# Kernel optimization log

Hardware: AMD Instinct MI355X
Metric: run time of the kernel (lower is better)

## Reference

```python
import jax, jax.numpy as jnp
import numpy as np

N, E, IN_DIM, HID, OUT = 50000, 800000, 256, 128, 128
EPS_BN = 1e-5
EPS_NORM = 1e-12


def leaky(x):
    return jnp.where(x >= 0, x, 0.2 * x)


def batchnorm(x, gamma, beta):
    # training-mode BatchNorm1d over node dimension
    mean = jnp.mean(x, axis=0)
    var = jnp.var(x, axis=0)
    return gamma * (x - mean) * jax.lax.rsqrt(var + EPS_BN) + beta


def sage_conv(x, src, dst, W_l, b_l, W_r):
    # PyG SAGEConv (mean aggr): lin_l(mean_{j->i} x_j) + lin_r(x_i)
    msg = x[src]  # [E, D] gather
    agg = jax.ops.segment_sum(msg, dst, num_segments=N)
    cnt = jax.ops.segment_sum(jnp.ones((E,), x.dtype), dst, num_segments=N)
    agg = agg / jnp.maximum(cnt, 1.0)[:, None]
    return agg @ W_l + b_l + x @ W_r


def setup_inputs() -> dict:
    key = jax.random.key(0)
    ks = jax.random.split(key, 16)
    s = lambda fan_in: (2.0 / fan_in) ** 0.5
    return {
        "x": jax.random.normal(ks[0], (N, IN_DIM), jnp.float32),
        "edge_index": jax.random.randint(ks[1], (2, E), 0, N),
        "W_in": jax.random.normal(ks[2], (IN_DIM, HID), jnp.float32) * s(IN_DIM),
        "b_in": jnp.zeros((HID,), jnp.float32),
        "g1": jnp.ones((HID,), jnp.float32),
        "be1": jnp.zeros((HID,), jnp.float32),
        "Wl1": jax.random.normal(ks[3], (HID, HID), jnp.float32) * s(HID),
        "bl1": jnp.zeros((HID,), jnp.float32),
        "Wr1": jax.random.normal(ks[4], (HID, HID), jnp.float32) * s(HID),
        "Wl2": jax.random.normal(ks[5], (HID, OUT), jnp.float32) * s(HID),
        "bl2": jnp.zeros((OUT,), jnp.float32),
        "Wr2": jax.random.normal(ks[6], (HID, OUT), jnp.float32) * s(HID),
        "Wskip": jax.random.normal(ks[7], (HID, OUT), jnp.float32) * s(HID),
        "bskip": jnp.zeros((OUT,), jnp.float32),
        "g2": jnp.ones((OUT,), jnp.float32),
        "be2": jnp.zeros((OUT,), jnp.float32),
    }


def reference(x, edge_index, W_in, b_in, g1, be1, Wl1, bl1, Wr1, Wl2, bl2, Wr2, Wskip, bskip, g2, be2):
    src, dst = edge_index[0], edge_index[1]
    h = batchnorm(leaky(x @ W_in + b_in), g1, be1)
    skip = h
    h1 = leaky(sage_conv(h, src, dst, Wl1, bl1, Wr1))  # dropout = identity (eval)
    h2 = sage_conv(h1, src, dst, Wl2, bl2, Wr2)
    out = h2 + (skip @ Wskip + bskip)
    out = batchnorm(out, g2, be2)
    norm = jnp.sqrt(jnp.sum(out * out, axis=1, keepdims=True))
    return out / jnp.maximum(norm, EPS_NORM)
```

## Files before the change

### kernel.cpp

```cpp
#include <hip/hip_runtime.h>
#include <math.h>

#define N_NODES 50000
#define N_EDGES 800000
#define IN_DIM 256
#define HID 128
#define ZPITCH 384

typedef unsigned short u16;
typedef u16 u16x8 __attribute__((ext_vector_type(8)));
typedef u16 u16x2 __attribute__((ext_vector_type(2)));
typedef __bf16 bf16x8 __attribute__((ext_vector_type(8)));
typedef float f32x4 __attribute__((ext_vector_type(4)));

union F8 { u16x8 u; bf16x8 h; };

__device__ __forceinline__ u16 f2b(float f) {
    unsigned u = __builtin_bit_cast(unsigned, f);
    u = (u + 0x7FFFu + ((u >> 16) & 1u)) >> 16;
    return (u16)u;
}
__device__ __forceinline__ float b2f(u16 h) {
    unsigned u = ((unsigned)h) << 16;
    return __builtin_bit_cast(float, u);
}

template<int A_F32>
__device__ __forceinline__ F8 load_a(const void* base, size_t row, int P, int koff)
{
    F8 r;
    if (A_F32) {
        const float* p = (const float*)base + row * P + koff;
        float4 f0 = *reinterpret_cast<const float4*>(p);
        float4 f1 = *reinterpret_cast<const float4*>(p + 4);
        r.h[0] = (__bf16)f0.x; r.h[1] = (__bf16)f0.y;
        r.h[2] = (__bf16)f0.z; r.h[3] = (__bf16)f0.w;
        r.h[4] = (__bf16)f1.x; r.h[5] = (__bf16)f1.y;
        r.h[6] = (__bf16)f1.z; r.h[7] = (__bf16)f1.w;
    } else {
        r.u = *reinterpret_cast<const u16x8*>((const u16*)base + row * P + koff);
    }
    return r;
}

template<int LEAKY, int STATS, int OUT_BF16, int A_F32>
__global__ __launch_bounds__(256) void gemm_mfma(
    int M, const void* __restrict__ A, int P, int K,
    const u16* __restrict__ Wf,
    const float* __restrict__ bias0, const float* __restrict__ bias1,
    void* __restrict__ Cout, int CP,
    float* __restrict__ stats)
{
    const int t   = threadIdx.x;
    const int w   = t >> 6;
    const int l   = t & 63;
    const int l15 = l & 15;
    const int lg  = l >> 4;
    const int rb  = blockIdx.x * 64 + w * 16;

    int r0 = rb + l15;
    size_t r0c = (size_t)(r0 < M ? r0 : M - 1);
    const int ko = lg * 8;
    const u16* pb = Wf + l * 8;

    f32x4 acc[8];
#pragma unroll
    for (int j = 0; j < 8; ++j) acc[j] = 0.0f;

    F8 a0, b[8];
    a0 = load_a<A_F32>(A, r0c, P, ko);
#pragma unroll
    for (int j = 0; j < 8; ++j) b[j].u = *(const u16x8*)(pb + j * 512);

    const int NC = K >> 5;
    for (int c = 1; c < NC; ++c) {
        F8 na0, nb[8];
        na0 = load_a<A_F32>(A, r0c, P, c * 32 + ko);
#pragma unroll
        for (int j = 0; j < 8; ++j) nb[j].u = *(const u16x8*)(pb + c * 4096 + j * 512);
#pragma unroll
        for (int j = 0; j < 8; ++j)
            acc[j] = __builtin_amdgcn_mfma_f32_16x16x32_bf16(a0.h, b[j].h, acc[j], 0, 0, 0);
        a0 = na0;
#pragma unroll
        for (int j = 0; j < 8; ++j) b[j] = nb[j];
    }
#pragma unroll
    for (int j = 0; j < 8; ++j)
        acc[j] = __builtin_amdgcn_mfma_f32_16x16x32_bf16(a0.h, b[j].h, acc[j], 0, 0, 0);

    float bias_j[8];
#pragma unroll
    for (int j = 0; j < 8; ++j) {
        float bb = bias0[16 * j + l15];
        if (bias1) bb += bias1[16 * j + l15];
        bias_j[j] = bb;
    }

    float csum[8], csq[8];
#pragma unroll
    for (int j = 0; j < 8; ++j) { csum[j] = 0.f; csq[j] = 0.f; }

    {
        int rbase = rb + lg * 4;
#pragma unroll
        for (int r = 0; r < 4; ++r) {
            int row = rbase + r;
            bool ok = row < M;
#pragma unroll
            for (int j = 0; j < 8; ++j) {
                float y = acc[j][r] + bias_j[j];
                if (LEAKY) y = (y >= 0.f) ? y : 0.2f * y;
                if (ok) {
                    if (OUT_BF16)
                        ((u16*)Cout)[(size_t)row * CP + 16 * j + l15] = f2b(y);
                    else
                        ((float*)Cout)[(size_t)row * CP + 16 * j + l15] = y;
                    if (STATS) { csum[j] += y; csq[j] += y * y; }
                }
            }
        }
    }

    if (STATS) {
        __shared__ float sred[256];
        sred[t] = 0.f;
        __syncthreads();
#pragma unroll
        for (int j = 0; j < 8; ++j) {
            float s = csum[j];
            float q = csq[j];
            s += __shfl_xor(s, 16); s += __shfl_xor(s, 32);
            q += __shfl_xor(q, 16); q += __shfl_xor(q, 32);
            if (lg == 0) {
                atomicAdd(&sred[16 * j + l15], s);
                atomicAdd(&sred[128 + 16 * j + l15], q);
            }
        }
        __syncthreads();
        atomicAdd(&stats[t], sred[t]);
    }
}

__global__ __launch_bounds__(256) void conv_w(const float* s0, const float* s1, const float* s2,
                                              const float* sc0, const float* sc1, const float* sc2,
                                              int rows_each, u16* __restrict__ dst, int nchunks)
{
    int tid = blockIdx.x * 256 + threadIdx.x;
    if (tid >= nchunks * 512) return;
    int c   = tid >> 9;
    int j   = (tid >> 6) & 7;
    int l   = tid & 63;
    int l15 = l & 15, lg = l >> 4;

    int srow0 = c * 32;
    int si    = srow0 / rows_each;
    const float* S  = (si == 0) ? s0 : (si == 1) ? s1 : s2;
    const float* SC = (si == 0) ? sc0 : (si == 1) ? sc1 : sc2;
    int rbase = srow0 - si * rows_each + lg * 8;
    int col   = 16 * j + l15;

    u16x8 o;
#pragma unroll
    for (int i = 0; i < 8; ++i) {
        float v = S[(size_t)(rbase + i) * HID + col];
        if (SC) v *= SC[rbase + i];
        o[i] = f2b(v);
    }
    reinterpret_cast<u16x8*>(dst)[tid] = o;
}

__global__ void bias_fold(const float* __restrict__ b0, const float* __restrict__ b1,
                          const float* __restrict__ W0, const float* __restrict__ W1,
                          const float* __restrict__ sh, float* __restrict__ outb)
{
    int j = threadIdx.x;
    float acc = b0[j] + (b1 ? b1[j] : 0.f);
    for (int i = 0; i < HID; ++i) {
        float w = W0[(size_t)i * HID + j] + (W1 ? W1[(size_t)i * HID + j] : 0.f);
        acc = fmaf(sh[i], w, acc);
    }
    outb[j] = acc;
}

__global__ void bn_params(const float* __restrict__ stats,
                          const float* __restrict__ gamma,
                          const float* __restrict__ beta,
                          float* __restrict__ scale,
                          float* __restrict__ shift, float invn)
{
    int j = threadIdx.x;
    float mean = stats[j] * invn;
    float var  = stats[128 + j] * invn - mean * mean;
    var = fmaxf(var, 0.f);
    float sc = gamma[j] / sqrtf(var + 1e-5f);
    scale[j] = sc;
    shift[j] = beta[j] - mean * sc;
}

__global__ __launch_bounds__(256) void edge_count(const int* __restrict__ dst, int* __restrict__ cnt)
{
    int e = blockIdx.x * 256 + threadIdx.x;
    if (e < N_EDGES) atomicAdd(&cnt[dst[e]], 1);
}

__global__ __launch_bounds__(256) void scan_block(const int* __restrict__ cnt,
                                                  int* __restrict__ excl,
                                                  int* __restrict__ bsum, int n)
{
    __shared__ int sh[256];
    int t = threadIdx.x;
    int i = blockIdx.x * 256 + t;
    int v = (i < n) ? cnt[i] : 0;
    sh[t] = v;
    __syncthreads();
#pragma unroll
    for (int off = 1; off < 256; off <<= 1) {
        int x = (t >= off) ? sh[t - off] : 0;
        __syncthreads();
        sh[t] += x;
        __syncthreads();
    }
    if (i < n) excl[i] = sh[t] - v;
    if (t == 255) bsum[blockIdx.x] = sh[255];
}

__global__ __launch_bounds__(256) void scan_bsum(int* __restrict__ bsum, int nb)
{
    __shared__ int sh[256];
    int t = threadIdx.x;
    int v = (t < nb) ? bsum[t] : 0;
    sh[t] = v;
    __syncthreads();
#pragma unroll
    for (int off = 1; off < 256; off <<= 1) {
        int x = (t >= off) ? sh[t - off] : 0;
        __syncthreads();
        sh[t] += x;
        __syncthreads();
    }
    if (t < nb) bsum[t] = sh[t] - v;
}

__global__ __launch_bounds__(256) void scan_add(int* __restrict__ row_ptr,
                                                int* __restrict__ fillrp,
                                                const int* __restrict__ bsum, int n)
{
    int i = blockIdx.x * 256 + threadIdx.x;
    if (i < n) {
        int v = row_ptr[i] + bsum[i >> 8];
        row_ptr[i] = v;
        fillrp[i]  = v;
    }
    if (i == 0) row_ptr[n] = N_EDGES;
}

#define FILL_EPB 4096
__global__ __launch_bounds__(256) void edge_fill_part(const int* __restrict__ src,
                                                      const int* __restrict__ dst,
                                                      int* __restrict__ fillrp,
                                                      int* __restrict__ col_idx)
{
    const int range = blockIdx.x & 7;
    const int base  = (blockIdx.x >> 3) * FILL_EPB;
    const int lo = range * 6250, hi = lo + 6250;
#pragma unroll
    for (int k = 0; k < FILL_EPB / 256; ++k) {
        int e = base + k * 256 + threadIdx.x;
        if (e < N_EDGES) {
            int d = dst[e];
            if (d >= lo && d < hi) {
                int pos = atomicAdd(&fillrp[d], 1);
                col_idx[pos] = src[e];
            }
        }
    }
}

__global__ __launch_bounds__(256) void spmm_mean(const int* __restrict__ row_ptr,
                                                 const int* __restrict__ col_idx,
                                                 const u16* __restrict__ Z_in,
                                                 u16* __restrict__ Z_out)
{
    int node = blockIdx.x * 4 + (threadIdx.x >> 6);
    if (node >= N_NODES) return;
    int lane = threadIdx.x & 63;
    int beg = row_ptr[node];
    int end = row_ptr[node + 1];

    float sx = 0.f, sy = 0.f;
    int e = beg;
    for (; e + 4 <= end; e += 4) {
        int c0 = col_idx[e], c1 = col_idx[e + 1], c2 = col_idx[e + 2], c3 = col_idx[e + 3];
        u16x2 v0 = *reinterpret_cast<const u16x2*>(Z_in + (size_t)c0 * ZPITCH + lane * 2);
        u16x2 v1 = *reinterpret_cast<const u16x2*>(Z_in + (size_t)c1 * ZPITCH + lane * 2);
        u16x2 v2 = *reinterpret_cast<const u16x2*>(Z_in + (size_t)c2 * ZPITCH + lane * 2);
        u16x2 v3 = *reinterpret_cast<const u16x2*>(Z_in + (size_t)c3 * ZPITCH + lane * 2);
        sx += (b2f(v0[0]) + b2f(v1[0])) + (b2f(v2[0]) + b2f(v3[0]));
        sy += (b2f(v0[1]) + b2f(v1[1])) + (b2f(v2[1]) + b2f(v3[1]));
    }
    for (; e < end; ++e) {
        int c = col_idx[e];
        u16x2 v = *reinterpret_cast<const u16x2*>(Z_in + (size_t)c * ZPITCH + lane * 2);
        sx += b2f(v[0]); sy += b2f(v[1]);
    }
    float inv = 1.f / fmaxf((float)(end - beg), 1.f);
    u16x2 r; r[0] = f2b(sx * inv); r[1] = f2b(sy * inv);
    *reinterpret_cast<u16x2*>(Z_out + (size_t)node * ZPITCH + lane * 2) = r;
}

__global__ __launch_bounds__(256) void bn_rownorm(float* __restrict__ out,
                                                  const float* __restrict__ scale,
                                                  const float* __restrict__ shift)
{
    int row = blockIdx.x * 4 + (threadIdx.x >> 6);
    if (row >= N_NODES) return;
    int lane = threadIdx.x & 63;
    float2 v  = *reinterpret_cast<const float2*>(&out[(size_t)row * HID + lane * 2]);
    float2 sc = *reinterpret_cast<const float2*>(&scale[lane * 2]);
    float2 sh = *reinterpret_cast<const float2*>(&shift[lane * 2]);
    float y0 = v.x * sc.x + sh.x;
    float y1 = v.y * sc.y + sh.y;
    float ss = y0 * y0 + y1 * y1;
#pragma unroll
    for (int m = 1; m < 64; m <<= 1) ss += __shfl_xor(ss, m);
    float inv = 1.f / fmaxf(sqrtf(ss), 1e-12f);
    float2 r = {y0 * inv, y1 * inv};
    *reinterpret_cast<float2*>(&out[(size_t)row * HID + lane * 2]) = r;
}

extern "C" void kernel_launch(void* const* d_in, const int* in_sizes, int n_in,
                              void* d_out, int out_size, void* d_ws, size_t ws_size,
                              hipStream_t stream)
{
    const float* x     = (const float*)d_in[0];
    const int*   ei    = (const int*)d_in[1];
    const float* W_in  = (const float*)d_in[2];
    const float* b_in  = (const float*)d_in[3];
    const float* g1    = (const float*)d_in[4];
    const float* be1   = (const float*)d_in[5];
    const float* Wl1   = (const float*)d_in[6];
    const float* bl1   = (const float*)d_in[7];
    const float* Wr1   = (const float*)d_in[8];
    const float* Wl2   = (const float*)d_in[9];
    const float* bl2   = (const float*)d_in[10];
    const float* Wr2   = (const float*)d_in[11];
    const float* Wskip = (const float*)d_in[12];
    const float* bskip = (const float*)d_in[13];
    const float* g2    = (const float*)d_in[14];
    const float* be2   = (const float*)d_in[15];
    float* out = (float*)d_out;

    char* ws = (char*)d_ws;
    u16*  Z  = (u16*)ws;
    char* zzone = ws + 38400000;
    float* stats = (float*)zzone;
    int*   icnt  = (int*)(zzone + 2048);
    size_t zsz   = 2048 + (size_t)N_NODES * 4;
    int*   row_ptr = (int*)(zzone + zsz);
    int*   fillrp  = (int*)(zzone + zsz + 200064);
    int*   bsum    = (int*)(zzone + zsz + 400128);
    int*   col_idx = (int*)(zzone + zsz + 400128 + 1024);
    float* bnc     = (float*)(zzone + zsz + 400128 + 1024 + (size_t)N_EDGES * 4);
    u16* WfA = (u16*)((char*)bnc + 4096);
    u16* WfB = WfA + 8 * 4096;
    u16* WfC = WfB + 8 * 4096;

    hipMemsetAsync(zzone, 0, zsz, stream);

    const int* srcp = ei;
    const int* dstp = ei + N_EDGES;

    float* scale1 = bnc;
    float* shift1 = bnc + 128;
    float* scale2 = bnc + 256;
    float* shift2 = bnc + 384;
    float* b1eff  = bnc + 512;
    float* b2eff  = bnc + 640;

    conv_w<<<16, 256, 0, stream>>>(W_in, nullptr, nullptr, nullptr, nullptr, nullptr,
                                   256, WfA, 8);

    const int NB = (N_NODES + 255) / 256;
    edge_count<<<(N_EDGES + 255) / 256, 256, 0, stream>>>(dstp, icnt);
    scan_block<<<NB, 256, 0, stream>>>(icnt, row_ptr, bsum, N_NODES);
    scan_bsum<<<1, 256, 0, stream>>>(bsum, NB);
    scan_add<<<NB, 256, 0, stream>>>(row_ptr, fillrp, bsum, N_NODES);
    edge_fill_part<<<((N_EDGES + FILL_EPB - 1) / FILL_EPB) * 8, 256, 0, stream>>>(
        srcp, dstp, fillrp, col_idx);

    const int GB = (N_NODES + 63) / 64;

    gemm_mfma<1, 1, 1, 1><<<GB, 256, 0, stream>>>(
        N_NODES, x, IN_DIM, 256, WfA, b_in, nullptr, Z + 128, ZPITCH, stats);
    bn_params<<<1, 128, 0, stream>>>(stats, g1, be1, scale1, shift1, 1.f / N_NODES);

    conv_w<<<16, 256, 0, stream>>>(Wl1, Wr1, nullptr, scale1, scale1, nullptr,
                                   128, WfB, 8);
    conv_w<<<24, 256, 0, stream>>>(Wl2, Wskip, Wr2, nullptr, scale1, nullptr,
                                   128, WfC, 12);
    bias_fold<<<1, 128, 0, stream>>>(bl1, nullptr, Wl1, Wr1, shift1, b1eff);
    bias_fold<<<1, 128, 0, stream>>>(bl2, bskip, Wskip, nullptr, shift1, b2eff);

    spmm_mean<<<(N_NODES + 3) / 4, 256, 0, stream>>>(row_ptr, col_idx, Z + 128, Z);
    gemm_mfma<1, 0, 1, 0><<<GB, 256, 0, stream>>>(
        N_NODES, Z, ZPITCH, 256, WfB, b1eff, nullptr, Z + 256, ZPITCH, nullptr);

    spmm_mean<<<(N_NODES + 3) / 4, 256, 0, stream>>>(row_ptr, col_idx, Z + 256, Z);
    gemm_mfma<0, 1, 0, 0><<<GB, 256, 0, stream>>>(
        N_NODES, Z, ZPITCH, 384, WfC, b2eff, nullptr, out, HID, stats + 256);

    bn_params<<<1, 128, 0, stream>>>(stats + 256, g2, be2, scale2, shift2, 1.f / N_NODES);
    bn_rownorm<<<(N_NODES + 3) / 4, 256, 0, stream>>>(out, scale2, shift2);
}
```

Baseline: 314.9 us.

## Stage packed weights in LDS and preload all A fragments in MFMA GEMM

The GEMM kernel now copies the whole packed weight matrix into shared memory once per block, and each wave reads its B fragments from LDS instead of global memory. Blocks grow to 512 threads covering 128 rows, and the K-loop is unrolled at compile time with all A fragments loaded up front. This cuts redundant global and L2 reads of the weights and exposes more memory-level parallelism. The cost is up to 96KB of LDS and more registers, which may limit occupancy, plus a block-wide sync before compute.

```diff
diff --git a/kernel.cpp b/kernel.cpp
--- a/kernel.cpp
+++ b/kernel.cpp
@@ -43,51 +43,51 @@
     return r;
 }
 
-template<int LEAKY, int STATS, int OUT_BF16, int A_F32>
-__global__ __launch_bounds__(256) void gemm_mfma(
-    int M, const void* __restrict__ A, int P, int K,
+template<int LEAKY, int STATS, int OUT_BF16, int A_F32, int NC>
+__global__ __launch_bounds__(512, 3) void gemm_mfma(
+    int M, const void* __restrict__ A, int P,
     const u16* __restrict__ Wf,
     const float* __restrict__ bias0, const float* __restrict__ bias1,
     void* __restrict__ Cout, int CP,
     float* __restrict__ stats)
 {
+    __shared__ u16 Bs[NC * 4096];
+
     const int t   = threadIdx.x;
     const int w   = t >> 6;
     const int l   = t & 63;
     const int l15 = l & 15;
     const int lg  = l >> 4;
-    const int rb  = blockIdx.x * 64 + w * 16;
+    const int rb  = blockIdx.x * 128 + w * 16;
 
     int r0 = rb + l15;
     size_t r0c = (size_t)(r0 < M ? r0 : M - 1);
     const int ko = lg * 8;
-    const u16* pb = Wf + l * 8;
+
+    F8 a[NC];
+#pragma unroll
+    for (int c = 0; c < NC; ++c) a[c] = load_a<A_F32>(A, r0c, P, c * 32 + ko);
+
+#pragma unroll
+    for (int i = 0; i < NC; ++i) {
+        int idx = i * 512 + t;
+        reinterpret_cast<u16x8*>(Bs)[idx] = reinterpret_cast<const u16x8*>(Wf)[idx];
+    }
+    __syncthreads();
 
     f32x4 acc[8];
 #pragma unroll
     for (int j = 0; j < 8; ++j) acc[j] = 0.0f;
 
-    F8 a0, b[8];
-    a0 = load_a<A_F32>(A, r0c, P, ko);
-#pragma unroll
-    for (int j = 0; j < 8; ++j) b[j].u = *(const u16x8*)(pb + j * 512);
-
-    const int NC = K >> 5;
-    for (int c = 1; c < NC; ++c) {
-        F8 na0, nb[8];
-        na0 = load_a<A_F32>(A, r0c, P, c * 32 + ko);
-#pragma unroll
-        for (int j = 0; j < 8; ++j) nb[j].u = *(const u16x8*)(pb + c * 4096 + j * 512);
-#pragma unroll
-        for (int j = 0; j < 8; ++j)
-            acc[j] = __builtin_amdgcn_mfma_f32_16x16x32_bf16(a0.h, b[j].h, acc[j], 0, 0, 0);
-        a0 = na0;
-#pragma unroll
-        for (int j = 0; j < 8; ++j) b[j] = nb[j];
-    }
-#pragma unroll
-    for (int j = 0; j < 8; ++j)
-        acc[j] = __builtin_amdgcn_mfma_f32_16x16x32_bf16(a0.h, b[j].h, acc[j], 0, 0, 0);
+#pragma unroll
+    for (int c = 0; c < NC; ++c) {
+#pragma unroll
+        for (int j = 0; j < 8; ++j) {
+            F8 b;
+            b.u = reinterpret_cast<const u16x8*>(Bs)[(c * 8 + j) * 64 + l];
+            acc[j] = __builtin_amdgcn_mfma_f32_16x16x32_bf16(a[c].h, b.h, acc[j], 0, 0, 0);
+        }
+    }
 
     float bias_j[8];
 #pragma unroll
@@ -124,7 +124,7 @@
 
     if (STATS) {
         __shared__ float sred[256];
-        sred[t] = 0.f;
+        if (t < 256) sred[t] = 0.f;
         __syncthreads();
 #pragma unroll
         for (int j = 0; j < 8; ++j) {
@@ -138,7 +138,7 @@
             }
         }
         __syncthreads();
-        atomicAdd(&stats[t], sred[t]);
+        if (t < 256) atomicAdd(&stats[t], sred[t]);
     }
 }
 
@@ -389,10 +389,10 @@
     edge_fill_part<<<((N_EDGES + FILL_EPB - 1) / FILL_EPB) * 8, 256, 0, stream>>>(
         srcp, dstp, fillrp, col_idx);
 
-    const int GB = (N_NODES + 63) / 64;
-
-    gemm_mfma<1, 1, 1, 1><<<GB, 256, 0, stream>>>(
-        N_NODES, x, IN_DIM, 256, WfA, b_in, nullptr, Z + 128, ZPITCH, stats);
+    const int GB = (N_NODES + 127) / 128;
+
+    gemm_mfma<1, 1, 1, 1, 8><<<GB, 512, 0, stream>>>(
+        N_NODES, x, IN_DIM, WfA, b_in, nullptr, Z + 128, ZPITCH, stats);
     bn_params<<<1, 128, 0, stream>>>(stats, g1, be1, scale1, shift1, 1.f / N_NODES);
 
     conv_w<<<16, 256, 0, stream>>>(Wl1, Wr1, nullptr, scale1, scale1, nullptr,
@@ -403,12 +403,12 @@
     bias_fold<<<1, 128, 0, stream>>>(bl2, bskip, Wskip, nullptr, shift1, b2eff);
 
     spmm_mean<<<(N_NODES + 3) / 4, 256, 0, stream>>>(row_ptr, col_idx, Z + 128, Z);
-    gemm_mfma<1, 0, 1, 0><<<GB, 256, 0, stream>>>(
-        N_NODES, Z, ZPITCH, 256, WfB, b1eff, nullptr, Z + 256, ZPITCH, nullptr);
+    gemm_mfma<1, 0, 1, 0, 8><<<GB, 512, 0, stream>>>(
+        N_NODES, Z, ZPITCH, WfB, b1eff, nullptr, Z + 256, ZPITCH, nullptr);
 
     spmm_mean<<<(N_NODES + 3) / 4, 256, 0, stream>>>(row_ptr, col_idx, Z + 256, Z);
-    gemm_mfma<0, 1, 0, 0><<<GB, 256, 0, stream>>>(
-        N_NODES, Z, ZPITCH, 384, WfC, b2eff, nullptr, out, HID, stats + 256);
+    gemm_mfma<0, 1, 0, 0, 12><<<GB, 512, 0, stream>>>(
+        N_NODES, Z, ZPITCH, WfC, b2eff, nullptr, out, HID, stats + 256);
 
     bn_params<<<1, 128, 0, stream>>>(stats + 256, g2, be2, scale2, shift2, 1.f / N_NODES);
     bn_rownorm<<<(N_NODES + 3) / 4, 256, 0, stream>>>(out, scale2, shift2);
```

Measured after the change: 276.2 us. -12.3%, faster.
